# Performance work log

Measured on AMD Instinct MI355X. Metric: run time of the kernel, lower is better.

## Reference

```python
import jax, jax.numpy as jnp
import numpy as np

N_NODES = 50000
N_EDGES = 800000
C = 16          # in = hidden = out channels
FE = 8          # num_edge_features
NUM_GRAPHS = 64


def _nnconv(x, src, dst, edge_attr, w_e, b_e, root, bias):
    # edge MLP -> per-edge weight matrix [E, Cin, Cout]
    cin = x.shape[1]
    W = (edge_attr @ w_e + b_e).reshape(-1, cin, root.shape[1])
    msg = jnp.einsum('ei,eio->eo', x[src], W)            # gather + per-edge matvec
    n = x.shape[0]
    agg = jax.ops.segment_sum(msg, dst, num_segments=n)  # scatter-add
    cnt = jax.ops.segment_sum(jnp.ones((msg.shape[0], 1), x.dtype), dst, num_segments=n)
    agg = agg / jnp.maximum(cnt, 1.0)                    # aggr='mean'
    return x @ root + agg + bias


def setup_inputs() -> dict:
    key = jax.random.key(0)
    ks = jax.random.split(key, 12)
    x = jax.random.normal(ks[0], (N_NODES, C), dtype=jnp.float32)
    edge_index = jax.random.randint(ks[1], (2, N_EDGES), 0, N_NODES, dtype=jnp.int64)
    edge_attr = jax.random.uniform(ks[2], (N_EDGES, FE), dtype=jnp.float32)
    batch = jnp.sort(jax.random.randint(ks[3], (N_NODES,), 0, NUM_GRAPHS, dtype=jnp.int64))
    s = 1.0 / np.sqrt(C)
    se = 1.0 / np.sqrt(FE)
    we1 = jax.random.normal(ks[4], (FE, C * C), dtype=jnp.float32) * se
    be1 = jnp.zeros((C * C,), dtype=jnp.float32)
    root1 = jax.random.normal(ks[5], (C, C), dtype=jnp.float32) * s
    bias1 = jnp.zeros((C,), dtype=jnp.float32)
    we2 = jax.random.normal(ks[6], (FE, C * C), dtype=jnp.float32) * se
    be2 = jnp.zeros((C * C,), dtype=jnp.float32)
    root2 = jax.random.normal(ks[7], (C, C), dtype=jnp.float32) * s
    bias2 = jnp.zeros((C,), dtype=jnp.float32)
    return {"x": x, "edge_index": edge_index, "edge_attr": edge_attr, "batch": batch,
            "we1": we1, "be1": be1, "root1": root1, "bias1": bias1,
            "we2": we2, "be2": be2, "root2": root2, "bias2": bias2}


def reference(x, edge_index, edge_attr, batch,
              we1, be1, root1, bias1, we2, be2, root2, bias2):
    src, dst = edge_index[0], edge_index[1]
    # layer 1 (activation=None -> identity; dropout_prob=0 -> identity)
    h = _nnconv(x, src, dst, edge_attr, we1, be1, root1, bias1)
    # layer 2
    h = _nnconv(h, src, dst, edge_attr, we2, be2, root2, bias2)
    # global mean pool per graph, then flatten
    sums = jax.ops.segment_sum(h, batch, num_segments=NUM_GRAPHS)
    cnts = jax.ops.segment_sum(jnp.ones((h.shape[0], 1), h.dtype), batch, num_segments=NUM_GRAPHS)
    pooled = sums / jnp.maximum(cnts, 1.0)
    return pooled.reshape(-1)
```

## Files before the change

### kernel.cpp

```cpp
#include <hip/hip_runtime.h>

#define NN 50000
#define NE 800000
#define NG 64
#define NB ((NN + 255) / 256)
#define WROW 193

__global__ __launch_bounds__(256) void histk(const int* __restrict__ dst,
                                             int* __restrict__ deg) {
    int e = blockIdx.x * 256 + threadIdx.x;
    if (e < NE) atomicAdd(&deg[dst[e]], 1);
}

__global__ __launch_bounds__(256) void bsumk(const int* __restrict__ deg,
                                             int* __restrict__ bsum) {
    int idx = blockIdx.x * 256 + threadIdx.x;
    int v = (idx < NN) ? deg[idx] : 0;
#pragma unroll
    for (int off = 32; off > 0; off >>= 1) v += __shfl_down(v, off);
    __shared__ int ws[4];
    int lane = threadIdx.x & 63, w = threadIdx.x >> 6;
    if (lane == 0) ws[w] = v;
    __syncthreads();
    if (threadIdx.x == 0) bsum[blockIdx.x] = ws[0] + ws[1] + ws[2] + ws[3];
}

__global__ __launch_bounds__(256) void bscank(const int* __restrict__ bsum,
                                              int* __restrict__ boffs) {
    int tid = threadIdx.x;
    int v = (tid < NB) ? bsum[tid] : 0;
    int lane = tid & 63, w = tid >> 6;
    int t = v;
#pragma unroll
    for (int off = 1; off < 64; off <<= 1) {
        int u = __shfl_up(t, off);
        if (lane >= off) t += u;
    }
    __shared__ int ws[4];
    if (lane == 63) ws[w] = t;
    __syncthreads();
    int add = 0;
    for (int k = 0; k < w; k++) add += ws[k];
    if (tid < NB) boffs[tid] = add + t - v;
}

__global__ __launch_bounds__(256) void fscank(const int* __restrict__ deg,
                                              const int* __restrict__ boffs,
                                              int* __restrict__ row,
                                              int* __restrict__ cur) {
    int idx = blockIdx.x * 256 + threadIdx.x;
    int v = (idx < NN) ? deg[idx] : 0;
    int lane = threadIdx.x & 63, w = threadIdx.x >> 6;
    int t = v;
#pragma unroll
    for (int off = 1; off < 64; off <<= 1) {
        int u = __shfl_up(t, off);
        if (lane >= off) t += u;
    }
    __shared__ int ws[4];
    if (lane == 63) ws[w] = t;
    __syncthreads();
    int add = boffs[blockIdx.x];
    for (int k = 0; k < w; k++) add += ws[k];
    int ex = add + t - v;
    if (idx < NN) { row[idx] = ex; cur[idx] = ex; }
    else if (idx == NN) row[NN] = ex;
}

__global__ __launch_bounds__(256) void scatk(const int* __restrict__ src,
                                             const int* __restrict__ dst,
                                             const float* __restrict__ ea,
                                             int* __restrict__ cur,
                                             float* __restrict__ rec) {
    int e = blockIdx.x * 256 + threadIdx.x;
    if (e >= NE) return;
    int d = dst[e];
    int pos = atomicAdd(&cur[d], 1);
    float4 a = *(const float4*)(ea + (size_t)e * 8);
    float4 b = *(const float4*)(ea + (size_t)e * 8 + 4);
    float4* r = (float4*)(rec + (size_t)pos * 16);
    float4 r0; r0.x = __int_as_float(src[e]); r0.y = a.x; r0.z = a.y; r0.w = a.z;
    float4 r1; r1.x = a.w; r1.y = b.x; r1.z = b.y; r1.w = b.z;
    float4 r2; r2.x = b.w; r2.y = 0.f; r2.z = 0.f; r2.w = 0.f;
    float4 r3; r3.x = 0.f; r3.y = 0.f; r3.z = 0.f; r3.w = 0.f;
    r[0] = r0; r[1] = r1; r[2] = r2; r[3] = r3;
}

template <bool POOL>
__global__ __launch_bounds__(256) void fusedk(const float* __restrict__ xin,
                                              const int* __restrict__ row,
                                              const float* __restrict__ rec,
                                              const float* __restrict__ we,
                                              const float* __restrict__ be,
                                              const float* __restrict__ root,
                                              const float* __restrict__ bias,
                                              const int* __restrict__ batch,
                                              float* __restrict__ out,
                                              float* __restrict__ gsum,
                                              float* __restrict__ gcnt) {
    __shared__ float wlds[16 * WROW];
    __shared__ float bs[16];
    __shared__ float gacc[16][16];
    __shared__ int gcnta[16];
    int tid = threadIdx.x;
    for (int idx = tid; idx < 2048; idx += 256) {
        int f = idx >> 8, rest = idx & 255, i = rest >> 4, o = rest & 15;
        wlds[i * WROW + o * 12 + f] = we[idx];
    }
    {
        int i = tid >> 4, o = tid & 15;
        wlds[i * WROW + o * 12 + 8] = be[tid];
        wlds[i * WROW + o * 12 + 9] = root[tid];
    }
    if (tid < 16) bs[tid] = bias[tid];
    if (POOL) {
        gacc[tid >> 4][tid & 15] = 0.f;
        if (tid < 16) gcnta[tid] = 0;
    }
    __syncthreads();

    int g = tid >> 4, t = tid & 15;
    int v = blockIdx.x * 16 + g;
    int r0 = row[v], r1 = row[v + 1];

    float p0 = 0.f, p1 = 0.f, p2 = 0.f, p3 = 0.f;
    float p4 = 0.f, p5 = 0.f, p6 = 0.f, p7 = 0.f, s = 0.f;

    int pos = r0;
    int pend = r0 + ((r1 - r0) & ~3);
    for (; pos < pend; pos += 4) {
        const float* q0 = rec + (size_t)(pos + 0) * 16;
        const float* q1 = rec + (size_t)(pos + 1) * 16;
        const float* q2 = rec + (size_t)(pos + 2) * 16;
        const float* q3 = rec + (size_t)(pos + 3) * 16;
        float4 a0 = *(const float4*)q0; float4 b0 = *(const float4*)(q0 + 4); float e0 = q0[8];
        float4 a1 = *(const float4*)q1; float4 b1 = *(const float4*)(q1 + 4); float e1 = q1[8];
        float4 a2 = *(const float4*)q2; float4 b2 = *(const float4*)(q2 + 4); float e2 = q2[8];
        float4 a3 = *(const float4*)q3; float4 b3 = *(const float4*)(q3 + 4); float e3 = q3[8];
        float x0 = xin[(size_t)__float_as_int(a0.x) * 16 + t];
        float x1 = xin[(size_t)__float_as_int(a1.x) * 16 + t];
        float x2 = xin[(size_t)__float_as_int(a2.x) * 16 + t];
        float x3 = xin[(size_t)__float_as_int(a3.x) * 16 + t];
        p0 += a0.y * x0; p1 += a0.z * x0; p2 += a0.w * x0; p3 += b0.x * x0;
        p4 += b0.y * x0; p5 += b0.z * x0; p6 += b0.w * x0; p7 += e0 * x0; s += x0;
        p0 += a1.y * x1; p1 += a1.z * x1; p2 += a1.w * x1; p3 += b1.x * x1;
        p4 += b1.y * x1; p5 += b1.z * x1; p6 += b1.w * x1; p7 += e1 * x1; s += x1;
        p0 += a2.y * x2; p1 += a2.z * x2; p2 += a2.w * x2; p3 += b2.x * x2;
        p4 += b2.y * x2; p5 += b2.z * x2; p6 += b2.w * x2; p7 += e2 * x2; s += x2;
        p0 += a3.y * x3; p1 += a3.z * x3; p2 += a3.w * x3; p3 += b3.x * x3;
        p4 += b3.y * x3; p5 += b3.z * x3; p6 += b3.w * x3; p7 += e3 * x3; s += x3;
    }
    for (; pos < r1; ++pos) {
        const float* q = rec + (size_t)pos * 16;
        float4 a = *(const float4*)q; float4 b = *(const float4*)(q + 4); float e8 = q[8];
        float xv = xin[(size_t)__float_as_int(a.x) * 16 + t];
        p0 += a.y * xv; p1 += a.z * xv; p2 += a.w * xv; p3 += b.x * xv;
        p4 += b.y * xv; p5 += b.z * xv; p6 += b.w * xv; p7 += e8 * xv; s += xv;
    }

    int dg = r1 - r0;
    float inv = 1.0f / (float)(dg > 1 ? dg : 1);
    float xv = xin[(size_t)v * 16 + t];

    float a[16];
    const float* wr = wlds + t * WROW;
#pragma unroll
    for (int o = 0; o < 16; o++) {
        const float* w = wr + o * 12;
        float agg = w[0] * p0 + w[1] * p1 + w[2] * p2 + w[3] * p3 +
                    w[4] * p4 + w[5] * p5 + w[6] * p6 + w[7] * p7 + w[8] * s;
        a[o] = agg * inv + w[9] * xv;
    }

    {
        int bit = (t >> 3) & 1;
#pragma unroll
        for (int k = 0; k < 8; k++) {
            float snd = bit ? a[k] : a[k + 8];
            float kp  = bit ? a[k + 8] : a[k];
            a[k] = kp + __shfl_xor(snd, 8);
        }
        bit = (t >> 2) & 1;
#pragma unroll
        for (int k = 0; k < 4; k++) {
            float snd = bit ? a[k] : a[k + 4];
            float kp  = bit ? a[k + 4] : a[k];
            a[k] = kp + __shfl_xor(snd, 4);
        }
        bit = (t >> 1) & 1;
#pragma unroll
        for (int k = 0; k < 2; k++) {
            float snd = bit ? a[k] : a[k + 2];
            float kp  = bit ? a[k + 2] : a[k];
            a[k] = kp + __shfl_xor(snd, 2);
        }
        bit = t & 1;
        {
            float snd = bit ? a[0] : a[1];
            float kp  = bit ? a[1] : a[0];
            a[0] = kp + __shfl_xor(snd, 1);
        }
    }
    float h = a[0] + bs[t];

    if (!POOL) {
        out[(size_t)v * 16 + t] = h;
    } else {
        int bmin = batch[blockIdx.x * 16];
        int b = batch[v];
        int slot = b - bmin;
        if (slot < 16) {
            atomicAdd(&gacc[slot][t], h);
            if (t == 0) atomicAdd(&gcnta[slot], 1);
        } else {
            atomicAdd(&gsum[(size_t)b * 16 + t], h);
            if (t == 0) atomicAdd(&gcnt[b], 1.0f);
        }
        __syncthreads();
        if (gcnta[g] > 0) {
            atomicAdd(&gsum[(size_t)(bmin + g) * 16 + t], gacc[g][t]);
            if (t == 0) atomicAdd(&gcnt[bmin + g], (float)gcnta[g]);
        }
    }
}

__global__ void fink(const float* __restrict__ gsum,
                     const float* __restrict__ gcnt,
                     float* __restrict__ out) {
    int i = blockIdx.x * 256 + threadIdx.x;
    if (i < NG * 16) out[i] = gsum[i] / fmaxf(gcnt[i >> 4], 1.0f);
}

extern "C" void kernel_launch(void* const* d_in, const int* in_sizes, int n_in,
                              void* d_out, int out_size, void* d_ws, size_t ws_size,
                              hipStream_t stream) {
    const float* x     = (const float*)d_in[0];
    const int*   ei    = (const int*)d_in[1];
    const float* ea    = (const float*)d_in[2];
    const int*   batch = (const int*)d_in[3];
    const float* we1   = (const float*)d_in[4];
    const float* be1   = (const float*)d_in[5];
    const float* root1 = (const float*)d_in[6];
    const float* bias1 = (const float*)d_in[7];
    const float* we2   = (const float*)d_in[8];
    const float* be2   = (const float*)d_in[9];
    const float* root2 = (const float*)d_in[10];
    const float* bias2 = (const float*)d_in[11];

    float* ws = (float*)d_ws;
    float* rec  = ws;
    float* h1   = rec + (size_t)NE * 16;
    int*   row  = (int*)(h1 + (size_t)NN * 16);
    int*   cur  = row + NN + 1;
    int*   deg  = cur + NN;
    int*   bsum = deg + NN;
    int*   boffs= bsum + NB;
    float* gsum = (float*)(boffs + NB);
    float* gcnt = gsum + NG * 16;

    hipMemsetAsync(deg, 0, (size_t)(NN + 2 * NB + NG * 16 + NG) * 4, stream);

    const int* src = ei;
    const int* dst = ei + NE;

    int gE = (NE + 255) / 256;
    int gV = NN / 16;

    histk<<<gE, 256, 0, stream>>>(dst, deg);
    bsumk<<<NB, 256, 0, stream>>>(deg, bsum);
    bscank<<<1, 256, 0, stream>>>(bsum, boffs);
    fscank<<<NB, 256, 0, stream>>>(deg, boffs, row, cur);
    scatk<<<gE, 256, 0, stream>>>(src, dst, ea, cur, rec);

    fusedk<false><<<gV, 256, 0, stream>>>(x, row, rec, we1, be1, root1, bias1,
                                          batch, h1, gsum, gcnt);
    fusedk<true><<<gV, 256, 0, stream>>>(h1, row, rec, we2, be2, root2, bias2,
                                         batch, h1 , gsum, gcnt);

    fink<<<4, 256, 0, stream>>>(gsum, gcnt, (float*)d_out);
}
```

Measured before the change: 190.4 us.

## Sort nodes by in-degree to balance per-block edge work in fused kernel

Adds a degree counting-sort (histogram, scan, scatter) that builds a node order grouped by in-degree, and the fused NNConv kernel now processes nodes in that order so the 16 nodes in a block have similar edge counts. This targets load imbalance and divergence, where short nodes sit idle while a long node in the same block finishes. Pooling moves to a separate kernel because blocks no longer hold contiguous nodes, and layer 2 now writes a separate h2 buffer. The cost is three extra small kernels, an extra pass over h2, and scattered output writes and row lookups.

```diff
diff --git a/kernel.cpp b/kernel.cpp
--- a/kernel.cpp
+++ b/kernel.cpp
@@ -5,6 +5,7 @@
 #define NG 64
 #define NB ((NN + 255) / 256)
 #define WROW 193
+#define NDB 512
 
 __global__ __launch_bounds__(256) void histk(const int* __restrict__ dst,
                                              int* __restrict__ deg) {
@@ -65,6 +66,45 @@
     int ex = add + t - v;
     if (idx < NN) { row[idx] = ex; cur[idx] = ex; }
     else if (idx == NN) row[NN] = ex;
+}
+
+__global__ __launch_bounds__(256) void dhistk(const int* __restrict__ deg,
+                                              int* __restrict__ dh) {
+    int v = blockIdx.x * 256 + threadIdx.x;
+    if (v < NN) {
+        int d = deg[v]; if (d > NDB - 1) d = NDB - 1;
+        atomicAdd(&dh[d], 1);
+    }
+}
+
+__global__ __launch_bounds__(512) void dscank(const int* __restrict__ dh,
+                                              int* __restrict__ dcur) {
+    int tid = threadIdx.x;
+    int v = dh[tid];
+    int lane = tid & 63, w = tid >> 6;
+    int t = v;
+#pragma unroll
+    for (int off = 1; off < 64; off <<= 1) {
+        int u = __shfl_up(t, off);
+        if (lane >= off) t += u;
+    }
+    __shared__ int ws[8];
+    if (lane == 63) ws[w] = t;
+    __syncthreads();
+    int add = 0;
+    for (int k = 0; k < w; k++) add += ws[k];
+    dcur[tid] = add + t - v;
+}
+
+__global__ __launch_bounds__(256) void dscatk(const int* __restrict__ deg,
+                                              int* __restrict__ dcur,
+                                              int* __restrict__ order) {
+    int v = blockIdx.x * 256 + threadIdx.x;
+    if (v < NN) {
+        int d = deg[v]; if (d > NDB - 1) d = NDB - 1;
+        int pos = atomicAdd(&dcur[d], 1);
+        order[pos] = v;
+    }
 }
 
 __global__ __launch_bounds__(256) void scatk(const int* __restrict__ src,
@@ -86,22 +126,17 @@
     r[0] = r0; r[1] = r1; r[2] = r2; r[3] = r3;
 }
 
-template <bool POOL>
 __global__ __launch_bounds__(256) void fusedk(const float* __restrict__ xin,
                                               const int* __restrict__ row,
                                               const float* __restrict__ rec,
+                                              const int* __restrict__ order,
                                               const float* __restrict__ we,
                                               const float* __restrict__ be,
                                               const float* __restrict__ root,
                                               const float* __restrict__ bias,
-                                              const int* __restrict__ batch,
-                                              float* __restrict__ out,
-                                              float* __restrict__ gsum,
-                                              float* __restrict__ gcnt) {
+                                              float* __restrict__ out) {
     __shared__ float wlds[16 * WROW];
     __shared__ float bs[16];
-    __shared__ float gacc[16][16];
-    __shared__ int gcnta[16];
     int tid = threadIdx.x;
     for (int idx = tid; idx < 2048; idx += 256) {
         int f = idx >> 8, rest = idx & 255, i = rest >> 4, o = rest & 15;
@@ -113,14 +148,10 @@
         wlds[i * WROW + o * 12 + 9] = root[tid];
     }
     if (tid < 16) bs[tid] = bias[tid];
-    if (POOL) {
-        gacc[tid >> 4][tid & 15] = 0.f;
-        if (tid < 16) gcnta[tid] = 0;
-    }
     __syncthreads();
 
     int g = tid >> 4, t = tid & 15;
-    int v = blockIdx.x * 16 + g;
+    int v = order[blockIdx.x * 16 + g];
     int r0 = row[v], r1 = row[v + 1];
 
     float p0 = 0.f, p1 = 0.f, p2 = 0.f, p3 = 0.f;
@@ -201,26 +232,36 @@
             a[0] = kp + __shfl_xor(snd, 1);
         }
     }
-    float h = a[0] + bs[t];
-
-    if (!POOL) {
-        out[(size_t)v * 16 + t] = h;
+    out[(size_t)v * 16 + t] = a[0] + bs[t];
+}
+
+__global__ __launch_bounds__(256) void poolk(const float* __restrict__ h2,
+                                             const int* __restrict__ batch,
+                                             float* __restrict__ gsum,
+                                             float* __restrict__ gcnt) {
+    __shared__ float gacc[16][16];
+    __shared__ int gcnta[16];
+    int tid = threadIdx.x;
+    gacc[tid >> 4][tid & 15] = 0.f;
+    if (tid < 16) gcnta[tid] = 0;
+    __syncthreads();
+    int g = tid >> 4, t = tid & 15;
+    int v = blockIdx.x * 16 + g;
+    float h = h2[(size_t)v * 16 + t];
+    int bmin = batch[blockIdx.x * 16];
+    int b = batch[v];
+    int slot = b - bmin;
+    if (slot < 16) {
+        atomicAdd(&gacc[slot][t], h);
+        if (t == 0) atomicAdd(&gcnta[slot], 1);
     } else {
-        int bmin = batch[blockIdx.x * 16];
-        int b = batch[v];
-        int slot = b - bmin;
-        if (slot < 16) {
-            atomicAdd(&gacc[slot][t], h);
-            if (t == 0) atomicAdd(&gcnta[slot], 1);
-        } else {
-            atomicAdd(&gsum[(size_t)b * 16 + t], h);
-            if (t == 0) atomicAdd(&gcnt[b], 1.0f);
-        }
-        __syncthreads();
-        if (gcnta[g] > 0) {
-            atomicAdd(&gsum[(size_t)(bmin + g) * 16 + t], gacc[g][t]);
-            if (t == 0) atomicAdd(&gcnt[bmin + g], (float)gcnta[g]);
-        }
+        atomicAdd(&gsum[(size_t)b * 16 + t], h);
+        if (t == 0) atomicAdd(&gcnt[b], 1.0f);
+    }
+    __syncthreads();
+    if (gcnta[g] > 0) {
+        atomicAdd(&gsum[(size_t)(bmin + g) * 16 + t], gacc[g][t]);
+        if (t == 0) atomicAdd(&gcnt[bmin + g], (float)gcnta[g]);
     }
 }
 
@@ -250,15 +291,20 @@
     float* ws = (float*)d_ws;
     float* rec  = ws;
     float* h1   = rec + (size_t)NE * 16;
-    int*   row  = (int*)(h1 + (size_t)NN * 16);
+    float* h2   = h1 + (size_t)NN * 16;
+    int*   order= (int*)(h2 + (size_t)NN * 16);
+    int*   row  = order + NN;
     int*   cur  = row + NN + 1;
     int*   deg  = cur + NN;
     int*   bsum = deg + NN;
     int*   boffs= bsum + NB;
-    float* gsum = (float*)(boffs + NB);
+    int*   dh   = boffs + NB;
+    int*   dcur = dh + NDB;
+    float* gsum = (float*)(dcur + NDB);
     float* gcnt = gsum + NG * 16;
 
-    hipMemsetAsync(deg, 0, (size_t)(NN + 2 * NB + NG * 16 + NG) * 4, stream);
+    hipMemsetAsync(deg, 0,
+                   (size_t)(NN + 2 * NB + 2 * NDB + NG * 16 + NG) * 4, stream);
 
     const int* src = ei;
     const int* dst = ei + NE;
@@ -270,12 +316,14 @@
     bsumk<<<NB, 256, 0, stream>>>(deg, bsum);
     bscank<<<1, 256, 0, stream>>>(bsum, boffs);
     fscank<<<NB, 256, 0, stream>>>(deg, boffs, row, cur);
+    dhistk<<<NB, 256, 0, stream>>>(deg, dh);
+    dscank<<<1, 512, 0, stream>>>(dh, dcur);
+    dscatk<<<NB, 256, 0, stream>>>(deg, dcur, order);
     scatk<<<gE, 256, 0, stream>>>(src, dst, ea, cur, rec);
 
-    fusedk<false><<<gV, 256, 0, stream>>>(x, row, rec, we1, be1, root1, bias1,
-                                          batch, h1, gsum, gcnt);
-    fusedk<true><<<gV, 256, 0, stream>>>(h1, row, rec, we2, be2, root2, bias2,
-                                         batch, h1 , gsum, gcnt);
+    fusedk<<<gV, 256, 0, stream>>>(x, row, rec, order, we1, be1, root1, bias1, h1);
+    fusedk<<<gV, 256, 0, stream>>>(h1, row, rec, order, we2, be2, root2, bias2, h2);
+    poolk<<<gV, 256, 0, stream>>>(h2, batch, gsum, gcnt);
 
     fink<<<4, 256, 0, stream>>>(gsum, gcnt, (float*)d_out);
 }
```

Result: slower. 493.1 us (+158.9%).
